# Kernel tuning notes

Hardware: AMD Instinct MI355X
Metric: run time of the kernel (lower is better)

The kernel has to match this reference:

```python
import jax, jax.numpy as jnp
import numpy as np

D_MODEL = 1024
NUM_HEADS = 16
THETA = 10000.0
NEG = -1000000.0  # masked_fill value used by the torch code


def _rope(x, token_positions, theta):
    # x: [B, H, S, d_head]; token_positions: [S] int
    d_k = x.shape[-1]
    half = d_k // 2
    j = jnp.arange(half, dtype=jnp.float32)
    inv_freq = theta ** (-(2.0 * j) / d_k)                      # [half]
    ang = token_positions.astype(jnp.float32)[:, None] * inv_freq  # [S, half]
    cos = jnp.cos(ang)
    sin = jnp.sin(ang)
    xp = x.reshape(x.shape[:-1] + (half, 2))  # adjacent pairs (pc, 2)
    x0, x1 = xp[..., 0], xp[..., 1]
    o0 = x0 * cos - x1 * sin
    o1 = x0 * sin + x1 * cos
    out = jnp.stack([o0, o1], axis=-1)
    return out.reshape(x.shape)


def setup_inputs() -> dict:
    key = jax.random.key(0)
    k0, k1, k2 = jax.random.split(key, 3)
    B, S, D = 2, 2048, D_MODEL
    std = (2.0 / (D + D)) ** 0.5
    X = jax.random.normal(k0, (B, S, D), dtype=jnp.float32)
    QKV_weights = jax.random.normal(k1, (3 * D, D), dtype=jnp.float32) * std
    O_weights = jax.random.normal(k2, (D, D), dtype=jnp.float32) * std
    token_positions = jnp.arange(S, dtype=jnp.int32)
    return {"X": X, "token_positions": token_positions,
            "QKV_weights": QKV_weights, "O_weights": O_weights}


def reference(X, token_positions, QKV_weights, O_weights):
    B, S, D = X.shape
    H = NUM_HEADS
    dh = D // H
    qkv = jnp.einsum('od,bsd->bso', QKV_weights, X)  # [B, S, 3D]
    Q, K, V = jnp.split(qkv, 3, axis=-1)

    def split_heads(t):
        return t.reshape(B, S, H, dh).transpose(0, 2, 1, 3)  # [B,H,S,dh]

    Q, K, V = split_heads(Q), split_heads(K), split_heads(V)
    Q = _rope(Q, token_positions, THETA)
    K = _rope(K, token_positions, THETA)

    scores = (jnp.einsum('bhqd,bhkd->bhqk', Q, K) / jnp.sqrt(jnp.float32(dh))).astype(jnp.float32)
    causal = jnp.tril(jnp.ones((S, S), dtype=bool))
    scores = jnp.where(causal, scores, NEG)
    probs = jax.nn.softmax(scores, axis=-1)
    attn = jnp.einsum('bhqk,bhkd->bhqd', probs, V.astype(jnp.float32)).astype(Q.dtype)
    attn = attn.transpose(0, 2, 1, 3).reshape(B, S, D)
    return jnp.einsum('od,bsd->bso', O_weights, attn)
```

## Files before the change

kernel.cpp:

```cpp
#include <hip/hip_runtime.h>
#include <math.h>

#define S_LEN 2048

using bf16x8  = __attribute__((ext_vector_type(8))) short;
using shortx4 = __attribute__((ext_vector_type(4))) short;
using f32x4   = __attribute__((ext_vector_type(4))) float;
using uintx4  = __attribute__((ext_vector_type(4))) unsigned;
using uintx2  = __attribute__((ext_vector_type(2))) unsigned;

static __device__ __forceinline__ short f2bf(float f) {
  unsigned u = __float_as_uint(f);
  u += 0x7fffu + ((u >> 16) & 1u);
  return (short)(u >> 16);
}

#if __has_builtin(__builtin_amdgcn_cvt_pk_bf16_f32)
using bf16x2_t = __attribute__((ext_vector_type(2))) __bf16;
static __device__ __forceinline__ unsigned pkbf(float a, float b) {
  bf16x2_t v = __builtin_amdgcn_cvt_pk_bf16_f32(a, b);
  return __builtin_bit_cast(unsigned, v);
}
#else
static __device__ __forceinline__ unsigned pkbf(float a, float b) {
  return (unsigned)(unsigned short)f2bf(a) | ((unsigned)(unsigned short)f2bf(b) << 16);
}
#endif

#define GLD_LDS16(gptr, lptr)                                                  \
  __builtin_amdgcn_global_load_lds(                                            \
      (__attribute__((address_space(1))) void*)(gptr),                         \
      (__attribute__((address_space(3))) void*)(lptr), 16, 0, 0)

#define EXP2_SHIFT 20.0f

static __device__ __forceinline__ f32x4 exp2s4(f32x4 a) {
  return (f32x4){__builtin_amdgcn_exp2f(a[0] - EXP2_SHIFT),
                 __builtin_amdgcn_exp2f(a[1] - EXP2_SHIFT),
                 __builtin_amdgcn_exp2f(a[2] - EXP2_SHIFT),
                 __builtin_amdgcn_exp2f(a[3] - EXP2_SHIFT)};
}

static __device__ __forceinline__ int sigma64(int k) {
  return (k & 0x20) | ((k & 0x0C) << 1) | ((k & 0x10) >> 2) | (k & 3);
}

__global__ __launch_bounds__(256) void init_kernel(const float* __restrict__ X,
                                                   const float* __restrict__ W1,
                                                   const float* __restrict__ W2,
                                                   const int* __restrict__ tok,
                                                   short* __restrict__ Xb,
                                                   short* __restrict__ W1b,
                                                   short* __restrict__ W2b,
                                                   float2* __restrict__ table) {
  if (blockIdx.x < 4096) {
    size_t idx = (size_t)(blockIdx.x * 256 + threadIdx.x) * 8;
    const float* src;
    short* dst;
    size_t off;
    if (idx < 4194304) { src = X; dst = Xb; off = idx; }
    else if (idx < 4194304 + 3145728) { src = W1; dst = W1b; off = idx - 4194304; }
    else { src = W2; dst = W2b; off = idx - (4194304 + 3145728); }
    float4 a = *(const float4*)(src + off);
    float4 b = *(const float4*)(src + off + 4);
    bf16x8 o = {f2bf(a.x), f2bf(a.y), f2bf(a.z), f2bf(a.w),
                f2bf(b.x), f2bf(b.y), f2bf(b.z), f2bf(b.w)};
    *(bf16x8*)(dst + off) = o;
  } else {
    int i = (blockIdx.x - 4096) * 256 + threadIdx.x;
    int s = i >> 5, j = i & 31;
    double pos = (double)tok[s];
    double ang = pos * pow(10000.0, -(double)j / 32.0);
    table[i] = make_float2((float)cos(ang), (float)sin(ang));
  }
}

template <int BM, typename OutT, int EPI>
__global__ __launch_bounds__(256) void gemm_ll(const short* __restrict__ A,
                                               const short* __restrict__ B,
                                               OutT* __restrict__ C,
                                               const float2* __restrict__ tab,
                                               short* __restrict__ Qb,
                                               short* __restrict__ Kb,
                                               short* __restrict__ VT,
                                               int M, int N, int K) {
  constexpr int MI = BM / 32;
  constexpr int AI = BM / 64;
  __shared__ short As[2][BM * 32];
  __shared__ short Bs[2][128 * 32];
  const int tid  = threadIdx.x;
  const int lane = tid & 63;
  const int wv   = tid >> 6;
  const int wm   = (wv >> 1) * (BM / 2);
  const int wn   = (wv & 1) * 64;
  const int m16  = lane & 15;
  const int q4   = lane >> 4;

  const int nwg = gridDim.x * gridDim.y;
  int bid = blockIdx.y * gridDim.x + blockIdx.x;
  bid = (bid & 7) * (nwg >> 3) + (bid >> 3);
  const int rowBase = (bid / gridDim.x) * BM;
  const int colBase = (bid % gridDim.x) * 128;

  const int lrow = lane >> 2;
  const int lchk = (lane & 3) ^ ((lane >> 3) & 3);
  const int fsw  = (q4 ^ ((m16 >> 1) & 3)) * 8;

  f32x4 acc[MI][4];
#pragma unroll
  for (int i = 0; i < MI; ++i)
#pragma unroll
    for (int j = 0; j < 4; ++j) acc[i][j] = (f32x4){0.f, 0.f, 0.f, 0.f};

  const short* ap[AI];
  const short* bp[2];
#pragma unroll
  for (int i = 0; i < AI; ++i)
    ap[i] = A + (size_t)(rowBase + (wv * AI + i) * 16 + lrow) * K + lchk * 8;
#pragma unroll
  for (int i = 0; i < 2; ++i)
    bp[i] = B + (size_t)(colBase + (wv * 2 + i) * 16 + lrow) * K + lchk * 8;

#define STAGE(buf)                                                             \
  do {                                                                         \
    _Pragma("unroll")                                                          \
    for (int i = 0; i < AI; ++i) {                                             \
      GLD_LDS16(ap[i], &As[buf][(wv * AI + i) * 512]);                         \
      ap[i] += 32;                                                             \
    }                                                                          \
    _Pragma("unroll")                                                          \
    for (int i = 0; i < 2; ++i) {                                              \
      GLD_LDS16(bp[i], &Bs[buf][(wv * 2 + i) * 512]);                          \
      bp[i] += 32;                                                             \
    }                                                                          \
  } while (0)

#define COMPUTE(buf)                                                           \
  do {                                                                         \
    bf16x8 af[MI], bfv[4];                                                     \
    _Pragma("unroll")                                                          \
    for (int mi = 0; mi < MI; ++mi)                                            \
      af[mi] = *(const bf16x8*)&As[buf][(wm + mi * 16 + m16) * 32 + fsw];      \
    _Pragma("unroll")                                                          \
    for (int ni = 0; ni < 4; ++ni)                                             \
      bfv[ni] = *(const bf16x8*)&Bs[buf][(wn + ni * 16 + m16) * 32 + fsw];     \
    __builtin_amdgcn_s_setprio(1);                                             \
    _Pragma("unroll")                                                          \
    for (int mi = 0; mi < MI; ++mi)                                            \
      _Pragma("unroll")                                                        \
      for (int ni = 0; ni < 4; ++ni)                                           \
        acc[mi][ni] = __builtin_amdgcn_mfma_f32_16x16x32_bf16(                 \
            af[mi], bfv[ni], acc[mi][ni], 0, 0, 0);                            \
    __builtin_amdgcn_s_setprio(0);                                             \
  } while (0)

  STAGE(0);
  __syncthreads();

  for (int kk = 0; kk < K; kk += 64) {
    STAGE(1);
    COMPUTE(0);
    __syncthreads();
    if (kk + 64 < K) STAGE(0);
    COMPUTE(1);
    __syncthreads();
  }
#undef STAGE
#undef COMPUTE

  if constexpr (EPI == 0) {
#pragma unroll
    for (int mi = 0; mi < MI; ++mi)
#pragma unroll
      for (int ni = 0; ni < 4; ++ni) {
        const int rbase = rowBase + wm + mi * 16 + q4 * 4;
        const int cidx  = colBase + wn + ni * 16 + m16;
#pragma unroll
        for (int r = 0; r < 4; ++r) {
          float v = acc[mi][ni][r];
          if constexpr (sizeof(OutT) == 2)
            C[(size_t)(rbase + r) * N + cidx] = (OutT)f2bf(v);
          else
            C[(size_t)(rbase + r) * N + cidx] = (OutT)v;
        }
      }
  } else {
    const int sect = colBase >> 10;
#pragma unroll
    for (int mi = 0; mi < MI; ++mi)
#pragma unroll
      for (int ni = 0; ni < 4; ++ni) {
        const int col = colBase + wn + ni * 16 + m16;
        const int rb  = rowBase + wm + mi * 16 + q4 * 4;
        if (sect == 2) {
          const int hd = col - 2048;
          const int h = hd >> 6, d = hd & 63;
          const int b = rb >> 11, s0 = rb & (S_LEN - 1);
          shortx4 pk4 = {f2bf(acc[mi][ni][0]), f2bf(acc[mi][ni][1]),
                         f2bf(acc[mi][ni][2]), f2bf(acc[mi][ni][3])};
          *(shortx4*)(VT + ((size_t)((b * 16 + h) * 64 + d)) * S_LEN +
                      (s0 & ~63) + sigma64(s0 & 63)) = pk4;
        } else {
          const int cc = col & 1023;
          const int h = cc >> 6, d = cc & 63, j = d >> 1;
          const float sgn = (m16 & 1) ? 1.f : -1.f;
          short* dstp = (sect == 0) ? Qb : Kb;
          const float scl = (sect == 0) ? (0.125f * 1.44269504f) : 1.f;
#pragma unroll
          for (int r = 0; r < 4; ++r) {
            const int row = rb + r;
            const int s = row & (S_LEN - 1), bidx = row >> 11;
            float2 cs = tab[s * 32 + j];
            float self = acc[mi][ni][r];
            float part = __shfl_xor(self, 1);
            float o = (self * cs.x + sgn * part * cs.y) * scl;
            dstp[((size_t)((bidx * 16 + h) * S_LEN + s)) * 64 + d] = f2bf(o);
          }
        }
      }
  }
}

__global__ __launch_bounds__(256, 2) void attn_mfma(const short* __restrict__ Qb,
                                                    const short* __restrict__ Kb,
                                                    const short* __restrict__ VT,
                                                    short* __restrict__ attnb) {
  __shared__ __align__(16) short Smem[18432];
  const int tid  = threadIdx.x;
  const int lane = tid & 63;
  const int w    = tid >> 6;
  const int m16  = lane & 15;
  const int q4   = lane >> 4;
  const int bh   = blockIdx.x;
  const int jtx  = blockIdx.y;
  const int jt   = (jtx < 8) ? (15 - jtx) : (jtx - 8);
  const int b    = bh >> 4, h = bh & 15;
  const short* Qh = Qb + (size_t)bh * S_LEN * 64;
  const short* Kh = Kb + (size_t)bh * S_LEN * 64;
  const short* Vh = VT + (size_t)bh * 64 * S_LEN;

  const int srow = tid >> 3;
  const int seg  = tid & 7;

  const bf16x8 ones = {16256, 16256, 16256, 16256, 16256, 16256, 16256, 16256};

  const int q0 = jt * 128;
  const int ktiles = 2 * jt + 2;

  bf16x8 qf[2][2];
#pragma unroll
  for (int n = 0; n < 2; ++n)
#pragma unroll
    for (int ks = 0; ks < 2; ++ks)
      qf[n][ks] = *(const bf16x8*)(Qh + (size_t)(q0 + w * 32 + n * 16 + m16) * 64 + ks * 32 + q4 * 8);

  f32x4 O[2][4], Lacc[2];
#pragma unroll
  for (int n = 0; n < 2; ++n) {
    Lacc[n] = (f32x4){0.f, 0.f, 0.f, 0.f};
#pragma unroll
    for (int c = 0; c < 4; ++c) O[n][c] = (f32x4){0.f, 0.f, 0.f, 0.f};
  }

  const short* kp[2];
  const short* vp[2];
#pragma unroll
  for (int i = 0; i < 2; ++i) {
    kp[i] = Kh + (size_t)(i * 32 + srow) * 64 + seg * 8;
    vp[i] = Vh + (size_t)(i * 32 + srow) * S_LEN + seg * 8;
  }

  bf16x8 kst[2], vst[2];
#pragma unroll
  for (int i = 0; i < 2; ++i) {
    kst[i] = *(const bf16x8*)kp[i];  kp[i] += 4096;
    vst[i] = *(const bf16x8*)vp[i];  vp[i] += 64;
  }

  for (int t = 0; t < ktiles; ++t) {
    short* Kc = Smem + (t & 1) * 9216;
    short* Vc = Kc + 64 * 72;
#pragma unroll
    for (int i = 0; i < 2; ++i) {
      *(bf16x8*)&Kc[(i * 32 + srow) * 72 + seg * 8] = kst[i];
      *(bf16x8*)&Vc[(i * 32 + srow) * 72 + seg * 8] = vst[i];
    }
    __syncthreads();

    if (t + 1 < ktiles) {
#pragma unroll
      for (int i = 0; i < 2; ++i) {
        kst[i] = *(const bf16x8*)kp[i];  kp[i] += 4096;
        vst[i] = *(const bf16x8*)vp[i];  vp[i] += 64;
      }
    }

    f32x4 sc[2][4];
#pragma unroll
    for (int n = 0; n < 2; ++n)
#pragma unroll
      for (int c = 0; c < 4; ++c) sc[n][c] = (f32x4){0.f, 0.f, 0.f, 0.f};
    __builtin_amdgcn_s_setprio(1);
#pragma unroll
    for (int ks = 0; ks < 2; ++ks) {
#pragma unroll
      for (int c = 0; c < 4; ++c) {
        bf16x8 kf = *(const bf16x8*)&Kc[(c * 16 + m16) * 72 + ks * 32 + q4 * 8];
#pragma unroll
        for (int n = 0; n < 2; ++n)
          sc[n][c] = __builtin_amdgcn_mfma_f32_16x16x32_bf16(kf, qf[n][ks], sc[n][c], 0, 0, 0);
      }
    }
    __builtin_amdgcn_s_setprio(0);

    if (t >= ktiles - 2) {
#pragma unroll
      for (int n = 0; n < 2; ++n)
#pragma unroll
        for (int c = 0; c < 4; ++c) {
          const int qg = q0 + w * 32 + n * 16 + m16;
#pragma unroll
          for (int rr = 0; rr < 4; ++rr) {
            const int kg = t * 64 + c * 16 + q4 * 4 + rr;
            if (kg > qg) sc[n][c][rr] = -1e30f;
          }
        }
    }

    bf16x8 pb[2][2];
#pragma unroll
    for (int n = 0; n < 2; ++n) {
#pragma unroll
      for (int c = 0; c < 4; ++c) sc[n][c] = exp2s4(sc[n][c]);
      uintx4 u0 = {pkbf(sc[n][0][0], sc[n][0][1]), pkbf(sc[n][0][2], sc[n][0][3]),
                   pkbf(sc[n][1][0], sc[n][1][1]), pkbf(sc[n][1][2], sc[n][1][3])};
      uintx4 u1 = {pkbf(sc[n][2][0], sc[n][2][1]), pkbf(sc[n][2][2], sc[n][2][3]),
                   pkbf(sc[n][3][0], sc[n][3][1]), pkbf(sc[n][3][2], sc[n][3][3])};
      pb[n][0] = __builtin_bit_cast(bf16x8, u0);
      pb[n][1] = __builtin_bit_cast(bf16x8, u1);
    }

    __builtin_amdgcn_s_setprio(1);
#pragma unroll
    for (int ch = 0; ch < 2; ++ch) {
#pragma unroll
      for (int c2 = 0; c2 < 4; ++c2) {
        bf16x8 va = *(const bf16x8*)&Vc[(c2 * 16 + m16) * 72 + ch * 32 + q4 * 8];
#pragma unroll
        for (int n = 0; n < 2; ++n)
          O[n][c2] = __builtin_amdgcn_mfma_f32_16x16x32_bf16(va, pb[n][ch], O[n][c2], 0, 0, 0);
      }
#pragma unroll
      for (int n = 0; n < 2; ++n)
        Lacc[n] = __builtin_amdgcn_mfma_f32_16x16x32_bf16(ones, pb[n][ch], Lacc[n], 0, 0, 0);
    }
    __builtin_amdgcn_s_setprio(0);
  }

#pragma unroll
  for (int n = 0; n < 2; ++n) {
    const float inv = __frcp_rn(Lacc[n][0]);
#pragma unroll
    for (int c2 = 0; c2 < 4; ++c2) {
      uintx2 uo = {pkbf(O[n][c2][0] * inv, O[n][c2][1] * inv),
                   pkbf(O[n][c2][2] * inv, O[n][c2][3] * inv)};
      *(shortx4*)&Smem[(w * 32 + n * 16 + m16) * 72 + c2 * 16 + q4 * 4] =
          __builtin_bit_cast(shortx4, uo);
    }
  }
  __syncthreads();
  {
    const int row = tid >> 1, hf = tid & 1;
    const short* src = &Smem[row * 72 + hf * 32];
    short* dst = attnb + (size_t)(b * S_LEN + q0 + row) * 1024 + h * 64 + hf * 32;
    ((bf16x8*)dst)[0] = ((const bf16x8*)src)[0];
    ((bf16x8*)dst)[1] = ((const bf16x8*)src)[1];
    ((bf16x8*)dst)[2] = ((const bf16x8*)src)[2];
    ((bf16x8*)dst)[3] = ((const bf16x8*)src)[3];
  }
}

extern "C" void kernel_launch(void* const* d_in, const int* in_sizes, int n_in,
                              void* d_out, int out_size, void* d_ws, size_t ws_size,
                              hipStream_t stream) {
  const float* X    = (const float*)d_in[0];
  const int*   tok  = (const int*)d_in[1];
  const float* Wqkv = (const float*)d_in[2];
  const float* Wo   = (const float*)d_in[3];
  float* out = (float*)d_out;

  char* w = (char*)d_ws;
  float2* table = (float2*)w;
  short*  Qb    = (short*)(w + 524288);
  short*  Kb    = Qb + 4194304;
  short*  VTt   = Kb + 4194304;
  short*  Xb    = VTt + 2 * 4194304;
  short*  Wqkvb = Xb + 4194304;
  short*  Wob   = Wqkvb + 3145728;
  short*  attnb = Wob + 1048576;

  hipLaunchKernelGGL(init_kernel, dim3(4352), dim3(256), 0, stream,
                     X, Wqkv, Wo, tok, Xb, Wqkvb, Wob, table);
  hipLaunchKernelGGL((gemm_ll<128, short, 1>), dim3(24, 32), dim3(256), 0, stream,
                     Xb, Wqkvb, (short*)nullptr, table, Qb, Kb, VTt, 4096, 3072, 1024);
  hipLaunchKernelGGL(attn_mfma, dim3(32, 16), dim3(256), 0, stream,
                     Qb, Kb, VTt, attnb);
  hipLaunchKernelGGL((gemm_ll<64, float, 0>), dim3(8, 64), dim3(256), 0, stream,
                     attnb, Wob, out, (const float2*)nullptr,
                     (short*)nullptr, (short*)nullptr, (short*)nullptr,
                     4096, 1024, 1024);
}
```

Before: 174.0 us.

## Deepen GEMM global-to-LDS pipeline to four stages with vmcnt-based waits

The projection GEMM moves from a double-buffered LDS scheme with two __syncthreads per 64-wide K step to a four-buffer ring. It keeps three 32-wide K stages in flight and gates each step with an explicit s_waitcnt vmcnt plus a single s_barrier. The aim is to hide more global-load latency and remove one block-wide barrier per step. The cost is doubled LDS use for the A/B tiles, which can lower occupancy. It also depends on the hand-counted vmcnt values matching the number of loads each stage issues.

```diff
diff --git a/kernel.cpp b/kernel.cpp
--- a/kernel.cpp
+++ b/kernel.cpp
@@ -31,6 +31,15 @@
   __builtin_amdgcn_global_load_lds(                                            \
       (__attribute__((address_space(1))) void*)(gptr),                         \
       (__attribute__((address_space(3))) void*)(lptr), 16, 0, 0)
+
+template <int N>
+static __device__ __forceinline__ void wait_vmcnt() {
+  if constexpr (N == 0)      asm volatile("s_waitcnt vmcnt(0)" ::: "memory");
+  else if constexpr (N == 3) asm volatile("s_waitcnt vmcnt(3)" ::: "memory");
+  else if constexpr (N == 4) asm volatile("s_waitcnt vmcnt(4)" ::: "memory");
+  else if constexpr (N == 6) asm volatile("s_waitcnt vmcnt(6)" ::: "memory");
+  else if constexpr (N == 8) asm volatile("s_waitcnt vmcnt(8)" ::: "memory");
+}
 
 #define EXP2_SHIFT 20.0f
 
@@ -84,10 +93,11 @@
                                                short* __restrict__ Kb,
                                                short* __restrict__ VT,
                                                int M, int N, int K) {
-  constexpr int MI = BM / 32;
-  constexpr int AI = BM / 64;
-  __shared__ short As[2][BM * 32];
-  __shared__ short Bs[2][128 * 32];
+  constexpr int MI  = BM / 32;
+  constexpr int AI  = BM / 64;
+  constexpr int LPS = AI + 2;
+  __shared__ short As[4][BM * 32];
+  __shared__ short Bs[4][128 * 32];
   const int tid  = threadIdx.x;
   const int lane = tid & 63;
   const int wv   = tid >> 6;
@@ -154,17 +164,25 @@
     __builtin_amdgcn_s_setprio(0);                                             \
   } while (0)
 
-  STAGE(0);
-  __syncthreads();
-
-  for (int kk = 0; kk < K; kk += 64) {
-    STAGE(1);
-    COMPUTE(0);
-    __syncthreads();
-    if (kk + 64 < K) STAGE(0);
-    COMPUTE(1);
-    __syncthreads();
-  }
+  const int NT = K >> 5;
+  STAGE(0); STAGE(1); STAGE(2);
+
+  int t = 0;
+  for (; t < NT - 2; ++t) {
+    wait_vmcnt<2 * LPS>();
+    __builtin_amdgcn_s_barrier();
+    __builtin_amdgcn_sched_barrier(0);
+    if (t + 3 < NT) STAGE((t + 3) & 3);
+    COMPUTE(t & 3);
+  }
+  wait_vmcnt<LPS>();
+  __builtin_amdgcn_s_barrier();
+  __builtin_amdgcn_sched_barrier(0);
+  COMPUTE((NT - 2) & 3);
+  wait_vmcnt<0>();
+  __builtin_amdgcn_s_barrier();
+  __builtin_amdgcn_sched_barrier(0);
+  COMPUTE((NT - 1) & 3);
 #undef STAGE
 #undef COMPUTE
 
```

After: 187.0 us. 1.07x slower.
